# Optimization experiments

Hardware: AMD Instinct MI355X
Metric: run time of the kernel (lower is better)

Reference implementation:

```python
import jax, jax.numpy as jnp
import numpy as np

M = 16384      # total flat points per role (8 scenes x 2048 pts)
D = 256        # d_model
H = 4          # heads
K = 16         # knn neighbors
DFF = 1024     # 4*D
LN_EPS = 1e-5


def _ln(x, g, b):
    m = jnp.mean(x, axis=-1, keepdims=True)
    v = jnp.mean((x - m) ** 2, axis=-1, keepdims=True)
    return (x - m) / jnp.sqrt(v + LN_EPS) * g + b


def _knn_block(x, coord, ctx, ctx_coord, idx,
               Wq, Wk, Wv, Wo, g1, b1, pe_w, pe_b,
               W1, bf1, W2, bf2, g2, b2):
    # x: [M,D] query feats; ctx: [N,D] context feats; idx: [M,K] neighbor ids (-1 = invalid)
    m, d = x.shape
    k = idx.shape[1]
    dh = d // H
    valid = idx >= 0
    idx_c = jnp.where(valid, idx, 0)

    xn = _ln(x, g1, b1)
    q = (xn @ Wq).reshape(m, H, dh)                      # [M,H,dh]
    k_all = ctx @ Wk                                     # [N,D]
    v_all = ctx @ Wv                                     # [N,D]

    rel = coord[:, None, :] - ctx_coord[idx_c]           # [M,K,3]
    pe = rel @ pe_w + pe_b                               # [M,K,D] relative position encoding
    kg = (k_all[idx_c] + pe).reshape(m, k, H, dh)        # gathered keys  [M,K,H,dh]
    vg = (v_all[idx_c] + pe).reshape(m, k, H, dh)        # gathered values

    scale = jnp.asarray(1.0 / np.sqrt(dh), x.dtype)
    scores = jnp.einsum('mhd,mkhd->mhk', q, kg) * scale
    scores = jnp.where(valid[:, None, :], scores, jnp.asarray(-1e9, x.dtype))
    attn = jax.nn.softmax(scores, axis=-1)
    out = jnp.einsum('mhk,mkhd->mhd', attn, vg).reshape(m, d) @ Wo
    x = x + out
    h = jax.nn.gelu(_ln(x, g2, b2) @ W1 + bf1)
    return x + (h @ W2 + bf2)


def setup_inputs() -> dict:
    key = jax.random.key(0)
    ks = jax.random.split(key, 24)
    s = 0.02
    nblk = 2  # [0]=self(a), [1]=cross(a,b)
    inp = {
        'feat_a': jax.random.normal(ks[0], (M, D), jnp.float32),
        'coord_a': jax.random.normal(ks[1], (M, 3), jnp.float32),
        'feat_b': jax.random.normal(ks[2], (M, D), jnp.float32),
        'coord_b': jax.random.normal(ks[3], (M, 3), jnp.float32),
        'Wq': jax.random.normal(ks[4], (nblk, D, D), jnp.float32) * s,
        'Wk': jax.random.normal(ks[5], (nblk, D, D), jnp.float32) * s,
        'Wv': jax.random.normal(ks[6], (nblk, D, D), jnp.float32) * s,
        'Wo': jax.random.normal(ks[7], (nblk, D, D), jnp.float32) * s,
        'ln1_g': jnp.ones((nblk, D), jnp.float32),
        'ln1_b': jnp.zeros((nblk, D), jnp.float32),
        'pe_w': jax.random.normal(ks[8], (nblk, 3, D), jnp.float32) * s,
        'pe_b': jnp.zeros((nblk, D), jnp.float32),
        'ffn_w1': jax.random.normal(ks[9], (nblk, D, DFF), jnp.float32) * s,
        'ffn_b1': jnp.zeros((nblk, DFF), jnp.float32),
        'ffn_w2': jax.random.normal(ks[10], (nblk, DFF, D), jnp.float32) * s,
        'ffn_b2': jnp.zeros((nblk, D), jnp.float32),
        'ln2_g': jnp.ones((nblk, D), jnp.float32),
        'ln2_b': jnp.zeros((nblk, D), jnp.float32),
        'knn_a2a': jax.random.randint(ks[11], (M, K), 0, M, jnp.int64 if jax.config.jax_enable_x64 else jnp.int32),
        'knn_a2b': jax.random.randint(ks[12], (M, K), 0, M, jnp.int64 if jax.config.jax_enable_x64 else jnp.int32),
    }
    return inp


def reference(feat_a, coord_a, feat_b, coord_b,
              Wq, Wk, Wv, Wo, ln1_g, ln1_b, pe_w, pe_b,
              ffn_w1, ffn_b1, ffn_w2, ffn_b2, ln2_g, ln2_b,
              knn_a2a, knn_a2b):
    def params(i):
        return (Wq[i], Wk[i], Wv[i], Wo[i], ln1_g[i], ln1_b[i], pe_w[i], pe_b[i],
                ffn_w1[i], ffn_b1[i], ffn_w2[i], ffn_b2[i], ln2_g[i], ln2_b[i])
    # layer 'self(a)': feat[a] = block(feat[a], coord[a], knn_indexes['a2a'])
    fa = _knn_block(feat_a, coord_a, feat_a, coord_a, knn_a2a, *params(0))
    # layer 'cross(a,b)': feat[a] = block(query=feat[a], context=feat[b], knn_indexes['a2b'])
    fa = _knn_block(fa, coord_a, feat_b, coord_b, knn_a2b, *params(1))
    return fa
```

## Files before the change

### kernel.cpp

```cpp
#include <hip/hip_runtime.h>
#include <hip/hip_bf16.h>
#include <stdint.h>

#define MM 16384
#define DD 256
#define HH 4
#define KK 16
#define DFF_ 1024

typedef __attribute__((ext_vector_type(8))) short bf16x8;
typedef __attribute__((ext_vector_type(16))) float f32x16;
typedef __attribute__((ext_vector_type(2))) float f32x2;

__device__ __forceinline__ unsigned short f2bf(float f) {
    unsigned u = __builtin_bit_cast(unsigned, f);
    unsigned r = u + 0x7fffu + ((u >> 16) & 1u);
    return (unsigned short)(r >> 16);
}
__device__ __forceinline__ float bf2f(unsigned short h) {
    unsigned u = ((unsigned)h) << 16;
    return __builtin_bit_cast(float, u);
}


__global__ __launch_bounds__(256) void prep_weights(
        const float* __restrict__ Wq, const float* __restrict__ Wk,
        const float* __restrict__ Wv, const float* __restrict__ Wo,
        const float* __restrict__ W1, const float* __restrict__ W2,
        unsigned short* __restrict__ wf) {
    int t = blockIdx.x * blockDim.x + threadIdx.x;
    const float* src; unsigned short* dst;
    int kd, lg, rem, blk, e, sect;
    if (t < 131072) { sect = 0; rem = t; blk = rem >> 16; e = rem & 65535;
        src = Wq; dst = wf + blk * 65536; kd = 256; lg = 8; }
    else if (t < 262144) { sect = 1; rem = t - 131072; blk = rem >> 16; e = rem & 65535;
        src = Wk; dst = wf + 131072 + blk * 131072; kd = 256; lg = 8; }
    else if (t < 393216) { sect = 2; rem = t - 262144; blk = rem >> 16; e = rem & 65535;
        src = Wv; dst = wf + 131072 + blk * 131072; kd = 256; lg = 8; }
    else if (t < 524288) { sect = 0; rem = t - 393216; blk = rem >> 16; e = rem & 65535;
        src = Wo; dst = wf + 393216 + blk * 65536; kd = 256; lg = 8; }
    else if (t < 1048576) { sect = 0; rem = t - 524288; blk = rem >> 18; e = rem & 262143;
        src = W1; dst = wf + 524288 + blk * 262144; kd = 256; lg = 10; }
    else if (t < 1572864) { sect = 0; rem = t - 1048576; blk = rem >> 18; e = rem & 262143;
        src = W2; dst = wf + 1048576 + blk * 262144; kd = 1024; lg = 8; }
    else return;
    int k = e >> lg;
    int n = e & ((1 << lg) - 1);
    if (sect == 1) n = (n >> 2) * 8 + (n & 3);
    else if (sect == 2) n = (n >> 2) * 8 + 4 + (n & 3);
    float v = src[(size_t)blk * kd * (1 << lg) + e];
    int off = ((n >> 5) * (kd >> 4) + (k >> 4)) * 512 + (((k >> 3) & 1) * 32 + (n & 31)) * 8 + (k & 7);
    dst[off] = f2bf(v);
}

__global__ __launch_bounds__(256) void ln3_to_frag(
        const float* __restrict__ xa, const float* __restrict__ g,
        const float* __restrict__ b, const float* __restrict__ xb,
        unsigned short* __restrict__ outln, unsigned short* __restrict__ outca,
        unsigned short* __restrict__ outcb) {
    int y = blockIdx.y;
    const float* x = (y == 2) ? xb : xa;
    unsigned short* out = (y == 0) ? outln : (y == 1 ? outca : outcb);
    int apply_ln = (y == 0);
    int wave = threadIdx.x >> 6, lane = threadIdx.x & 63;
    int m = blockIdx.x * 4 + wave;
    const float4 xv = reinterpret_cast<const float4*>(x + (size_t)m * DD)[lane];
    float vals[4] = {xv.x, xv.y, xv.z, xv.w};
    int k0 = lane * 4;
    if (apply_ln) {
        float s = vals[0] + vals[1] + vals[2] + vals[3];
        float sq = vals[0]*vals[0] + vals[1]*vals[1] + vals[2]*vals[2] + vals[3]*vals[3];
        for (int o = 32; o; o >>= 1) { s += __shfl_xor(s, o, 64); sq += __shfl_xor(sq, o, 64); }
        float mean = s * (1.0f / DD);
        float var = sq * (1.0f / DD) - mean * mean;
        float rs = rsqrtf(var + 1e-5f);
        #pragma unroll
        for (int c = 0; c < 4; ++c)
            vals[c] = (vals[c] - mean) * rs * g[k0 + c] + b[k0 + c];
    }
    int chunk = ((m >> 5) * (DD >> 4) + (k0 >> 4)) * 64 + ((k0 >> 3) & 1) * 32 + (m & 31);
    ushort4 o4 = make_ushort4(f2bf(vals[0]), f2bf(vals[1]), f2bf(vals[2]), f2bf(vals[3]));
    *reinterpret_cast<ushort4*>(out + (size_t)chunk * 8 + (k0 & 7)) = o4;
}

template <int KG>
__device__ __forceinline__ void compute_tile(
        const bf16x8* __restrict__ a0, const bf16x8* __restrict__ a1,
        const bf16x8* __restrict__ b0, const bf16x8* __restrict__ b1,
        f32x16 acc[2][2]) {
    #pragma unroll 4
    for (int g = 0; g < KG; ++g) {
        bf16x8 av0 = a0[g * 64];
        bf16x8 av1 = a1[g * 64];
        bf16x8 bv0 = b0[g * 64];
        bf16x8 bv1 = b1[g * 64];
        acc[0][0] = __builtin_amdgcn_mfma_f32_32x32x16_bf16(av0, bv0, acc[0][0], 0, 0, 0);
        acc[0][1] = __builtin_amdgcn_mfma_f32_32x32x16_bf16(av0, bv1, acc[0][1], 0, 0, 0);
        acc[1][0] = __builtin_amdgcn_mfma_f32_32x32x16_bf16(av1, bv0, acc[1][0], 0, 0, 0);
        acc[1][1] = __builtin_amdgcn_mfma_f32_32x32x16_bf16(av1, bv1, acc[1][1], 0, 0, 0);
    }
}

template <int O, int N>
__device__ __forceinline__ void redstage(float* a, int lane) {
    int sel = lane & O;
    #pragma unroll
    for (int u = 0; u < N / 2; ++u) {
        float lo = a[2 * u], hi = a[2 * u + 1];
        float keep = sel ? hi : lo;
        float send = sel ? lo : hi;
        a[u] = keep + __shfl_xor(send, O, 64);
    }
}

__global__ __launch_bounds__(512) void wo_ln_ffn1(
        const bf16x8* __restrict__ A, const bf16x8* __restrict__ Bo,
        float* __restrict__ xmid, const float* __restrict__ resid,
        const float* __restrict__ lng, const float* __restrict__ lnb,
        const bf16x8* __restrict__ B1, const float* __restrict__ b1,
        unsigned short* __restrict__ geluf) {
    constexpr int KG = 16;
    __shared__ float pstat[4][64][2];
    __shared__ float stats[64][2];
    __shared__ float tlds[8][32 * 33];
    __shared__ alignas(16) unsigned short xnlds[2][16][64][8];
    int wave = threadIdx.x >> 6, lane = threadIdx.x & 63;
    int wm = wave >> 2, wn = wave & 3;
    int m0 = blockIdx.x * 64;
    int mw = m0 + wm * 32;
    int n0 = wn * 64;
    const bf16x8* a0 = A + ((size_t)(mw >> 5) * KG) * 64 + lane;
    const bf16x8* b0 = Bo + ((size_t)(n0 >> 5) * KG) * 64 + lane;
    const bf16x8* b1o = b0 + (size_t)KG * 64;
    f32x16 acc[2] = {};
    #pragma unroll 4
    for (int g = 0; g < KG; ++g) {
        bf16x8 av = a0[g * 64];
        bf16x8 bv0 = b0[g * 64];
        bf16x8 bv1 = b1o[g * 64];
        acc[0] = __builtin_amdgcn_mfma_f32_32x32x16_bf16(av, bv0, acc[0], 0, 0, 0);
        acc[1] = __builtin_amdgcn_mfma_f32_32x32x16_bf16(av, bv1, acc[1], 0, 0, 0);
    }
    int col = lane & 31, rq = (lane >> 5) * 4;

    #pragma unroll
    for (int j = 0; j < 2; ++j) {
        #pragma unroll
        for (int r = 0; r < 16; ++r) {
            int row = (r & 3) + 8 * (r >> 2) + rq;
            int m = mw + row;
            int n = n0 + j * 32 + col;
            float v = acc[j][r];
            v += resid[(size_t)m * DD + n];
            xmid[(size_t)m * DD + n] = v;
            acc[j][r] = v;
        }
    }

    {
        float ps[16];
        #pragma unroll
        for (int r = 0; r < 16; ++r) ps[r] = acc[0][r] + acc[1][r];
        redstage<1, 16>(ps, lane);
        redstage<2, 8>(ps, lane);
        redstage<4, 4>(ps, lane);
        redstage<8, 2>(ps, lane);
        float sum64 = ps[0] + __shfl_xor(ps[0], 16, 64);
        float qs[16];
        #pragma unroll
        for (int r = 0; r < 16; ++r) {
            float a = acc[0][r], b = acc[1][r];
            qs[r] = a * a + b * b;
        }
        redstage<1, 16>(qs, lane);
        redstage<2, 8>(qs, lane);
        redstage<4, 4>(qs, lane);
        redstage<8, 2>(qs, lane);
        float sq64 = qs[0] + __shfl_xor(qs[0], 16, 64);
        int slot = lane & 15;
        int ROW = wm * 32 + (slot & 3) + 8 * (slot >> 2) + rq;
        if ((lane & 16) == 0)
            *reinterpret_cast<float2*>(&pstat[wn][ROW][0]) = make_float2(sum64, sq64);
    }
    __syncthreads();
    if (threadIdx.x < 64) {
        int R = threadIdx.x;
        float s = 0.0f, sq = 0.0f;
        #pragma unroll
        for (int w = 0; w < 4; ++w) {
            float2 p = *reinterpret_cast<float2*>(&pstat[w][R][0]);
            s += p.x; sq += p.y;
        }
        float mean = s * (1.0f / DD);
        float var = sq * (1.0f / DD) - mean * mean;
        float rstd = rsqrtf(var + 1e-5f);
        *reinterpret_cast<float2*>(&stats[R][0]) = make_float2(mean, rstd);
    }
    __syncthreads();

    {
        float* wlds = &tlds[wave][0];
        float mean_r[16], rstd_r[16];
        #pragma unroll
        for (int r = 0; r < 16; ++r) {
            int row = (r & 3) + 8 * (r >> 2) + rq;
            float2 st = *reinterpret_cast<float2*>(&stats[wm * 32 + row][0]);
            mean_r[r] = st.x; rstd_r[r] = st.y;
        }
        for (int j = 0; j < 2; ++j) {
            float gj = lng[n0 + j * 32 + col];
            float bj = lnb[n0 + j * 32 + col];
            #pragma unroll
            for (int r = 0; r < 16; ++r) {
                int row = (r & 3) + 8 * (r >> 2) + rq;
                float v = (acc[j][r] - mean_r[r]) * rstd_r[r] * gj + bj;
                wlds[row * 33 + col] = v;
            }
            #pragma unroll
            for (int it = 0; it < 2; ++it) {
                int task = lane + it * 64;
                int row = task >> 2, cc = task & 3;
                int m = mw + row;
                int k = n0 + j * 32 + cc * 8;
                float* p = &wlds[row * 33 + cc * 8];
                unsigned short us[8];
                #pragma unroll
                for (int e = 0; e < 8; ++e) us[e] = f2bf(p[e]);
                int lch = (k >> 4) * 64 + ((k >> 3) & 1) * 32 + (m & 31);
                reinterpret_cast<uint4*>(&xnlds[wm][0][0][0])[lch] = *reinterpret_cast<uint4*>(us);
            }
        }
    }
    __syncthreads();

    const bf16x8* la = (const bf16x8*)&xnlds[wm][0][0][0] + lane;
    #pragma unroll
    for (int h = 0; h < 2; ++h) {
        int nw3 = h * 512 + wn * 128;
        const bf16x8* bb = B1 + ((size_t)(nw3 >> 5) * KG) * 64 + lane;
        f32x16 acc4[4] = {};
        #pragma unroll 4
        for (int g = 0; g < KG; ++g) {
            bf16x8 av = la[g * 64];
            bf16x8 bv0 = bb[g * 64];
            bf16x8 bv1 = bb[(KG + g) * 64];
            bf16x8 bv2 = bb[(2 * KG + g) * 64];
            bf16x8 bv3 = bb[(3 * KG + g) * 64];
            acc4[0] = __builtin_amdgcn_mfma_f32_32x32x16_bf16(av, bv0, acc4[0], 0, 0, 0);
            acc4[1] = __builtin_amdgcn_mfma_f32_32x32x16_bf16(av, bv1, acc4[1], 0, 0, 0);
            acc4[2] = __builtin_amdgcn_mfma_f32_32x32x16_bf16(av, bv2, acc4[2], 0, 0, 0);
            acc4[3] = __builtin_amdgcn_mfma_f32_32x32x16_bf16(av, bv3, acc4[3], 0, 0, 0);
        }
        float* wlds = &tlds[wave][0];
        for (int j = 0; j < 4; ++j) {
            #pragma unroll
            for (int r = 0; r < 16; ++r) {
                int row = (r & 3) + 8 * (r >> 2) + rq;
                int n = nw3 + j * 32 + col;
                float v = acc4[j][r] + b1[n];
                float arg = v * (1.5957691216f + 0.0713548163f * v * v);
                v = v * __frcp_rn(1.0f + __expf(-arg));
                wlds[row * 33 + col] = v;
            }
            #pragma unroll
            for (int it = 0; it < 2; ++it) {
                int task = lane + it * 64;
                int row = task >> 2, cc = task & 3;
                int m = mw + row;
                int k = nw3 + j * 32 + cc * 8;
                float* p = &wlds[row * 33 + cc * 8];
                unsigned short us[8];
                #pragma unroll
                for (int e = 0; e < 8; ++e) us[e] = f2bf(p[e]);
                int chunk = ((m >> 5) * (DFF_ >> 4) + (k >> 4)) * 64 + ((k >> 3) & 1) * 32 + (m & 31);
                reinterpret_cast<uint4*>(geluf)[chunk] = *reinterpret_cast<uint4*>(us);
            }
        }
    }
}

template <int KD, int NOUT, bool RESID, bool BIAS>
__global__ __launch_bounds__(256) void gemm_frag64(
        const bf16x8* __restrict__ A, const bf16x8* __restrict__ B,
        float* __restrict__ outp, const float* __restrict__ resid,
        const float* __restrict__ bias) {
    constexpr int KG = KD / 16;
    int wave = threadIdx.x >> 6, lane = threadIdx.x & 63;
    int wm = wave & 1, wn = wave >> 1;
    int mw = blockIdx.x * 64 + wm * 32;
    int nw = blockIdx.y * 128 + wn * 64;
    const bf16x8* a0 = A + ((size_t)(mw >> 5) * KG) * 64 + lane;
    const bf16x8* b0 = B + ((size_t)(nw >> 5) * KG) * 64 + lane;
    const bf16x8* b1 = b0 + (size_t)KG * 64;
    f32x16 acc[2] = {};
    #pragma unroll 4
    for (int g = 0; g < KG; ++g) {
        bf16x8 av = a0[g * 64];
        bf16x8 bv0 = b0[g * 64];
        bf16x8 bv1 = b1[g * 64];
        acc[0] = __builtin_amdgcn_mfma_f32_32x32x16_bf16(av, bv0, acc[0], 0, 0, 0);
        acc[1] = __builtin_amdgcn_mfma_f32_32x32x16_bf16(av, bv1, acc[1], 0, 0, 0);
    }
    int col = lane & 31, rq = (lane >> 5) * 4;
    #pragma unroll
    for (int j = 0; j < 2; ++j) {
        #pragma unroll
        for (int r = 0; r < 16; ++r) {
            int row = (r & 3) + 8 * (r >> 2) + rq;
            int m = mw + row;
            int n = nw + j * 32 + col;
            float v = acc[j][r];
            if (BIAS) v += bias[n];
            if (RESID) v += resid[(size_t)m * NOUT + n];
            outp[(size_t)m * NOUT + n] = v;
        }
    }
}

__global__ __launch_bounds__(256) void gemm_qkv(
        const bf16x8* __restrict__ Aq, const bf16x8* __restrict__ Akv,
        const bf16x8* __restrict__ Bq, const bf16x8* __restrict__ Bkv,
        unsigned short* __restrict__ qout, unsigned char* __restrict__ kvout) {
    constexpr int KG = 16;
    int wave = threadIdx.x >> 6, lane = threadIdx.x & 63;
    int wm = wave & 1, wn = wave >> 1;
    int y = blockIdx.y;
    bool isQ = y < 2;
    const bf16x8* A = isQ ? Aq : Akv;
    const bf16x8* B = isQ ? Bq : Bkv;
    int n0 = (isQ ? y : y - 2) * 128 + wn * 64;
    int m0 = blockIdx.x * 128 + wm * 64;
    const bf16x8* a0 = A + ((size_t)(m0 >> 5) * KG) * 64 + lane;
    const bf16x8* a1 = a0 + (size_t)KG * 64;
    const bf16x8* b0 = B + ((size_t)(n0 >> 5) * KG) * 64 + lane;
    const bf16x8* b1 = b0 + (size_t)KG * 64;
    f32x16 acc[2][2] = {};
    compute_tile<KG>(a0, a1, b0, b1, acc);
    int col = lane & 31, rq = (lane >> 5) * 4;
    #pragma unroll
    for (int i = 0; i < 2; ++i)
    #pragma unroll
    for (int j = 0; j < 2; ++j)
    #pragma unroll
    for (int r = 0; r < 16; ++r) {
        int row = (r & 3) + 8 * (r >> 2) + rq;
        int m = m0 + i * 32 + row;
        int n = n0 + j * 32 + col;
        float v = acc[i][j][r];
        if (isQ) qout[(size_t)m * 256 + n] = f2bf(v);
        else kvout[(size_t)m * 512 + n] =
            (unsigned char)(__builtin_amdgcn_cvt_pk_fp8_f32(v, v, 0, false) & 0xff);
    }
}

template <int KD, bool BIAS>
__global__ __launch_bounds__(512) void gemm_ln(
        const bf16x8* __restrict__ A, const bf16x8* __restrict__ B,
        float* __restrict__ out_f32, const float* __restrict__ resid,
        const float* __restrict__ bias,
        const float* __restrict__ lng, const float* __restrict__ lnb,
        unsigned short* __restrict__ out_frag) {
    constexpr int KG = KD / 16;
    __shared__ float pstat[4][64][2];
    __shared__ float stats[64][2];
    __shared__ float tlds[8][32 * 33];
    int wave = threadIdx.x >> 6, lane = threadIdx.x & 63;
    int wm = wave >> 2, wn = wave & 3;
    int m0 = blockIdx.x * 64;
    int mw = m0 + wm * 32;
    int n0 = wn * 64;
    const bf16x8* a0 = A + ((size_t)(mw >> 5) * KG) * 64 + lane;
    const bf16x8* b0 = B + ((size_t)(n0 >> 5) * KG) * 64 + lane;
    const bf16x8* b1 = b0 + (size_t)KG * 64;
    f32x16 acc[2] = {};
    #pragma unroll 4
    for (int g = 0; g < KG; ++g) {
        bf16x8 av = a0[g * 64];
        bf16x8 bv0 = b0[g * 64];
        bf16x8 bv1 = b1[g * 64];
        acc[0] = __builtin_amdgcn_mfma_f32_32x32x16_bf16(av, bv0, acc[0], 0, 0, 0);
        acc[1] = __builtin_amdgcn_mfma_f32_32x32x16_bf16(av, bv1, acc[1], 0, 0, 0);
    }
    int col = lane & 31, rq = (lane >> 5) * 4;

    #pragma unroll
    for (int j = 0; j < 2; ++j) {
        #pragma unroll
        for (int r = 0; r < 16; ++r) {
            int row = (r & 3) + 8 * (r >> 2) + rq;
            int m = mw + row;
            int n = n0 + j * 32 + col;
            float v = acc[j][r];
            if (BIAS) v += bias[n];
            v += resid[(size_t)m * DD + n];
            out_f32[(size_t)m * DD + n] = v;
            acc[j][r] = v;
        }
    }

    {
        float ps[16];
        #pragma unroll
        for (int r = 0; r < 16; ++r)
            ps[r] = acc[0][r] + acc[1][r];
        redstage<1, 16>(ps, lane);
        redstage<2, 8>(ps, lane);
        redstage<4, 4>(ps, lane);
        redstage<8, 2>(ps, lane);
        float sum64 = ps[0] + __shfl_xor(ps[0], 16, 64);
        float qs[16];
        #pragma unroll
        for (int r = 0; r < 16; ++r) {
            float a = acc[0][r], b = acc[1][r];
            qs[r] = a * a + b * b;
        }
        redstage<1, 16>(qs, lane);
        redstage<2, 8>(qs, lane);
        redstage<4, 4>(qs, lane);
        redstage<8, 2>(qs, lane);
        float sq64 = qs[0] + __shfl_xor(qs[0], 16, 64);
        int slot = lane & 15;
        int ROW = wm * 32 + (slot & 3) + 8 * (slot >> 2) + rq;
        if ((lane & 16) == 0)
            *reinterpret_cast<float2*>(&pstat[wn][ROW][0]) = make_float2(sum64, sq64);
    }
    __syncthreads();
    if (threadIdx.x < 64) {
        int R = threadIdx.x;
        float s = 0.0f, sq = 0.0f;
        #pragma unroll
        for (int w = 0; w < 4; ++w) {
            float2 p = *reinterpret_cast<float2*>(&pstat[w][R][0]);
            s += p.x; sq += p.y;
        }
        float mean = s * (1.0f / DD);
        float var = sq * (1.0f / DD) - mean * mean;
        float rstd = rsqrtf(var + 1e-5f);
        *reinterpret_cast<float2*>(&stats[R][0]) = make_float2(mean, rstd);
    }
    __syncthreads();

    float* wlds = &tlds[wave][0];
    float mean_r[16], rstd_r[16];
    #pragma unroll
    for (int r = 0; r < 16; ++r) {
        int row = (r & 3) + 8 * (r >> 2) + rq;
        float2 st = *reinterpret_cast<float2*>(&stats[wm * 32 + row][0]);
        mean_r[r] = st.x; rstd_r[r] = st.y;
    }
    for (int j = 0; j < 2; ++j) {
        float gj = lng[n0 + j * 32 + col];
        float bj = lnb[n0 + j * 32 + col];
        #pragma unroll
        for (int r = 0; r < 16; ++r) {
            int row = (r & 3) + 8 * (r >> 2) + rq;
            float v = (acc[j][r] - mean_r[r]) * rstd_r[r] * gj + bj;
            wlds[row * 33 + col] = v;
        }
        #pragma unroll
        for (int it = 0; it < 2; ++it) {
            int task = lane + it * 64;
            int row = task >> 2, cc = task & 3;
            int m = mw + row;
            int k = n0 + j * 32 + cc * 8;
            float* p = &wlds[row * 33 + cc * 8];
            unsigned short us[8];
            #pragma unroll
            for (int e = 0; e < 8; ++e) us[e] = f2bf(p[e]);
            int chunk = ((m >> 5) * (DD >> 4) + (k >> 4)) * 64 + ((k >> 3) & 1) * 32 + (m & 31);
            *reinterpret_cast<uint4*>(out_frag + (size_t)chunk * 8) = *reinterpret_cast<uint4*>(us);
        }
    }
}

__global__ __launch_bounds__(256) void attn_kernel(
        const unsigned short* __restrict__ q, const unsigned char* __restrict__ kv,
        const float* __restrict__ coord, const float* __restrict__ ctx_coord,
        const int* __restrict__ knn,
        const float* __restrict__ pe_w, const float* __restrict__ pe_b,
        unsigned short* __restrict__ out_frag) {
    int wave = threadIdx.x >> 6, lane = threadIdx.x & 63;
    int m = blockIdx.x * 4 + wave;
    int s = lane & 15;
    int d0 = (lane >> 4) * 64 + s * 4;

    ushort4 qv4 = *reinterpret_cast<const ushort4*>(q + (size_t)m * DD + d0);
    float qx = bf2f(qv4.x), qy = bf2f(qv4.y), qz = bf2f(qv4.z), qw = bf2f(qv4.w);
    float4 pw0 = *reinterpret_cast<const float4*>(pe_w + d0);
    float4 pw1 = *reinterpret_cast<const float4*>(pe_w + DD + d0);
    float4 pw2 = *reinterpret_cast<const float4*>(pe_w + 2 * DD + d0);
    float4 pbv = *reinterpret_cast<const float4*>(pe_b + d0);

    float cx = coord[m * 3], cy = coord[m * 3 + 1], cz = coord[m * 3 + 2];
    int myidx = knn[(size_t)m * KK + s];
    int icm = myidx < 0 ? 0 : myidx;
    float rx = cx - ctx_coord[icm * 3];
    float ry = cy - ctx_coord[icm * 3 + 1];
    float rz = cz - ctx_coord[icm * 3 + 2];

    float t0 = qx * pw0.x + qy * pw0.y + qz * pw0.z + qw * pw0.w;
    float t1 = qx * pw1.x + qy * pw1.y + qz * pw1.z + qw * pw1.w;
    float t2 = qx * pw2.x + qy * pw2.y + qz * pw2.z + qw * pw2.w;
    float t3 = qx * pbv.x + qy * pbv.y + qz * pbv.z + qw * pbv.w;
// ... 63 lines not shown
    aw += wrx * pw0.w + wry * pw1.w + wrz * pw2.w + pbv.w;

    ushort4 o4 = make_ushort4(f2bf(ax), f2bf(ay), f2bf(az), f2bf(aw));
    int chunk = ((m >> 5) * (DD >> 4) + (d0 >> 4)) * 64 + ((d0 >> 3) & 1) * 32 + (m & 31);
    *reinterpret_cast<ushort4*>(out_frag + (size_t)chunk * 8 + (d0 & 7)) = o4;
}

extern "C" void kernel_launch(void* const* d_in, const int* in_sizes, int n_in,
                              void* d_out, int out_size, void* d_ws, size_t ws_size,
                              hipStream_t stream) {
    const float* feat_a = (const float*)d_in[0];
    const float* coord_a = (const float*)d_in[1];
    const float* feat_b = (const float*)d_in[2];
    const float* coord_b = (const float*)d_in[3];
    const float* Wq = (const float*)d_in[4];
    const float* Wk = (const float*)d_in[5];
    const float* Wv = (const float*)d_in[6];
    const float* Wo = (const float*)d_in[7];
    const float* ln1_g = (const float*)d_in[8];
    const float* ln1_b = (const float*)d_in[9];
    const float* pe_w = (const float*)d_in[10];
    const float* pe_b = (const float*)d_in[11];
    const float* W1 = (const float*)d_in[12];
    const float* b1 = (const float*)d_in[13];
    const float* W2 = (const float*)d_in[14];
    const float* b2 = (const float*)d_in[15];
    const float* ln2_g = (const float*)d_in[16];
    const float* ln2_b = (const float*)d_in[17];
    const int* knn_a2a = (const int*)d_in[18];
    const int* knn_a2b = (const int*)d_in[19];

    char* ws = (char*)d_ws;
    unsigned short* wfrag = (unsigned short*)ws;
    float* xmid = (float*)(ws + (4ull << 20));
    float* xout0 = (float*)(ws + (20ull << 20));
    unsigned short* qbuf = (unsigned short*)(ws + (36ull << 20));
    unsigned char* kvbuf = (unsigned char*)(ws + (52ull << 20));
    unsigned short* xnf = (unsigned short*)(ws + (68ull << 20));
    unsigned short* ctxfa = (unsigned short*)(ws + (76ull << 20));
    unsigned short* attnf = (unsigned short*)(ws + (84ull << 20));
    unsigned short* ctxfb = (unsigned short*)(ws + (92ull << 20));
    unsigned short* geluf = (unsigned short*)(ws + (36ull << 20));

    const unsigned short* WQF = wfrag;
    const unsigned short* KVF = wfrag + 131072;
    const unsigned short* WOF = wfrag + 393216;
    const unsigned short* W1F = wfrag + 524288;
    const unsigned short* W2F = wfrag + 1048576;

    prep_weights<<<(1572864 + 255) / 256, 256, 0, stream>>>(Wq, Wk, Wv, Wo, W1, W2, wfrag);

    ln3_to_frag<<<dim3(MM / 4, 3), 256, 0, stream>>>(feat_a, ln1_g, ln1_b, feat_b,
                                                     xnf, ctxfa, ctxfb);

    gemm_qkv<<<dim3(MM / 128, 6), 256, 0, stream>>>(
        (const bf16x8*)xnf, (const bf16x8*)ctxfa,
        (const bf16x8*)WQF, (const bf16x8*)KVF, qbuf, kvbuf);

    attn_kernel<<<MM / 4, 256, 0, stream>>>(qbuf, kvbuf, coord_a, coord_a, knn_a2a,
                                            pe_w, pe_b, attnf);

    wo_ln_ffn1<<<MM / 64, 512, 0, stream>>>(
        (const bf16x8*)attnf, (const bf16x8*)WOF, xmid, feat_a,
        ln2_g, ln2_b, (const bf16x8*)W1F, b1, geluf);

    gemm_ln<1024, true><<<MM / 64, 512, 0, stream>>>(
        (const bf16x8*)geluf, (const bf16x8*)W2F, xout0, xmid, b2,
        ln1_g + DD, ln1_b + DD, xnf);

    gemm_qkv<<<dim3(MM / 128, 6), 256, 0, stream>>>(
        (const bf16x8*)xnf, (const bf16x8*)ctxfb,
        (const bf16x8*)(WQF + 65536), (const bf16x8*)(KVF + 131072), qbuf, kvbuf);

    attn_kernel<<<MM / 4, 256, 0, stream>>>(qbuf, kvbuf, coord_a, coord_b, knn_a2b,
                                            pe_w + 3 * DD, pe_b + DD, attnf);

    wo_ln_ffn1<<<MM / 64, 512, 0, stream>>>(
        (const bf16x8*)attnf, (const bf16x8*)(WOF + 65536), xmid, xout0,
        ln2_g + DD, ln2_b + DD, (const bf16x8*)(W1F + 262144), b1 + DFF_, geluf);

    gemm_frag64<1024, 256, true, true><<<dim3(MM / 64, 2), 256, 0, stream>>>(
        (const bf16x8*)geluf, (const bf16x8*)(W2F + 262144), (float*)d_out, xmid,
        b2 + DD);
}
```

Measured before the change: 313.1 us.

## Fuse Wo, LN2, FFN1 and FFN2 into one kernel using FP8 FFN weights

Merges the Wo projection, residual add, LN2, the W1 GEMM with GELU, the W2 GEMM and the next block's LN1 into a single kernel per block. The GELU activations now stay in shared memory as FP8, so the global geluf and xmid round trips and two launches go away. The FFN weights are pre-quantised to FP8 with power-of-two scales and run through fp8 MFMA instructions. gemm_qkv also gets an XCD-aware block index remap. Risks include lower numerical precision from FP8, and heavy shared memory use (about 80 KB per block) that limits occupancy.

Result: faster. 292.9 us (-6.5%).

```diff
diff --git a/kernel.cpp b/kernel.cpp
--- a/kernel.cpp
+++ b/kernel.cpp
@@ -29,7 +29,7 @@
         const float* __restrict__ W1, const float* __restrict__ W2,
         unsigned short* __restrict__ wf) {
     int t = blockIdx.x * blockDim.x + threadIdx.x;
-    const float* src; unsigned short* dst;
+    const float* src; unsigned short* dst = nullptr;
     int kd, lg, rem, blk, e, sect;
     if (t < 131072) { sect = 0; rem = t; blk = rem >> 16; e = rem & 65535;
         src = Wq; dst = wf + blk * 65536; kd = 256; lg = 8; }
@@ -39,10 +39,10 @@
         src = Wv; dst = wf + 131072 + blk * 131072; kd = 256; lg = 8; }
     else if (t < 524288) { sect = 0; rem = t - 393216; blk = rem >> 16; e = rem & 65535;
         src = Wo; dst = wf + 393216 + blk * 65536; kd = 256; lg = 8; }
-    else if (t < 1048576) { sect = 0; rem = t - 524288; blk = rem >> 18; e = rem & 262143;
-        src = W1; dst = wf + 524288 + blk * 262144; kd = 256; lg = 10; }
-    else if (t < 1572864) { sect = 0; rem = t - 1048576; blk = rem >> 18; e = rem & 262143;
-        src = W2; dst = wf + 1048576 + blk * 262144; kd = 1024; lg = 8; }
+    else if (t < 1048576) { sect = 3; rem = t - 524288; blk = rem >> 18; e = rem & 262143;
+        src = W1; kd = 256; lg = 10; }
+    else if (t < 1572864) { sect = 4; rem = t - 1048576; blk = rem >> 18; e = rem & 262143;
+        src = W2; kd = 1024; lg = 8; }
     else return;
     int k = e >> lg;
     int n = e & ((1 << lg) - 1);
@@ -50,7 +50,17 @@
     else if (sect == 2) n = (n >> 2) * 8 + 4 + (n & 3);
     float v = src[(size_t)blk * kd * (1 << lg) + e];
     int off = ((n >> 5) * (kd >> 4) + (k >> 4)) * 512 + (((k >> 3) & 1) * 32 + (n & 31)) * 8 + (k & 7);
-    dst[off] = f2bf(v);
+    if (sect == 3) {
+        unsigned char* d8 = ((unsigned char*)wf) + 3145728 + blk * 262144;
+        float vs = v * 32.0f;
+        d8[off] = (unsigned char)(__builtin_amdgcn_cvt_pk_fp8_f32(vs, vs, 0, false) & 0xff);
+    } else if (sect == 4) {
+        unsigned char* d8 = ((unsigned char*)wf) + 3670016 + blk * 262144;
+        float vs = v * 16.0f;
+        d8[off] = (unsigned char)(__builtin_amdgcn_cvt_pk_fp8_f32(vs, vs, 0, false) & 0xff);
+    } else {
+        dst[off] = f2bf(v);
+    }
 }
 
 __global__ __launch_bounds__(256) void ln3_to_frag(
@@ -101,222 +111,6 @@
     }
 }
 
-template <int O, int N>
-__device__ __forceinline__ void redstage(float* a, int lane) {
-    int sel = lane & O;
-    #pragma unroll
-    for (int u = 0; u < N / 2; ++u) {
-        float lo = a[2 * u], hi = a[2 * u + 1];
-        float keep = sel ? hi : lo;
-        float send = sel ? lo : hi;
-        a[u] = keep + __shfl_xor(send, O, 64);
-    }
-}
-
-__global__ __launch_bounds__(512) void wo_ln_ffn1(
-        const bf16x8* __restrict__ A, const bf16x8* __restrict__ Bo,
-        float* __restrict__ xmid, const float* __restrict__ resid,
-        const float* __restrict__ lng, const float* __restrict__ lnb,
-        const bf16x8* __restrict__ B1, const float* __restrict__ b1,
-        unsigned short* __restrict__ geluf) {
-    constexpr int KG = 16;
-    __shared__ float pstat[4][64][2];
-    __shared__ float stats[64][2];
-    __shared__ float tlds[8][32 * 33];
-    __shared__ alignas(16) unsigned short xnlds[2][16][64][8];
-    int wave = threadIdx.x >> 6, lane = threadIdx.x & 63;
-    int wm = wave >> 2, wn = wave & 3;
-    int m0 = blockIdx.x * 64;
-    int mw = m0 + wm * 32;
-    int n0 = wn * 64;
-    const bf16x8* a0 = A + ((size_t)(mw >> 5) * KG) * 64 + lane;
-    const bf16x8* b0 = Bo + ((size_t)(n0 >> 5) * KG) * 64 + lane;
-    const bf16x8* b1o = b0 + (size_t)KG * 64;
-    f32x16 acc[2] = {};
-    #pragma unroll 4
-    for (int g = 0; g < KG; ++g) {
-        bf16x8 av = a0[g * 64];
-        bf16x8 bv0 = b0[g * 64];
-        bf16x8 bv1 = b1o[g * 64];
-        acc[0] = __builtin_amdgcn_mfma_f32_32x32x16_bf16(av, bv0, acc[0], 0, 0, 0);
-        acc[1] = __builtin_amdgcn_mfma_f32_32x32x16_bf16(av, bv1, acc[1], 0, 0, 0);
-    }
-    int col = lane & 31, rq = (lane >> 5) * 4;
-
-    #pragma unroll
-    for (int j = 0; j < 2; ++j) {
-        #pragma unroll
-        for (int r = 0; r < 16; ++r) {
-            int row = (r & 3) + 8 * (r >> 2) + rq;
-            int m = mw + row;
-            int n = n0 + j * 32 + col;
-            float v = acc[j][r];
-            v += resid[(size_t)m * DD + n];
-            xmid[(size_t)m * DD + n] = v;
-            acc[j][r] = v;
-        }
-    }
-
-    {
-        float ps[16];
-        #pragma unroll
-        for (int r = 0; r < 16; ++r) ps[r] = acc[0][r] + acc[1][r];
-        redstage<1, 16>(ps, lane);
-        redstage<2, 8>(ps, lane);
-        redstage<4, 4>(ps, lane);
-        redstage<8, 2>(ps, lane);
-        float sum64 = ps[0] + __shfl_xor(ps[0], 16, 64);
-        float qs[16];
-        #pragma unroll
-        for (int r = 0; r < 16; ++r) {
-            float a = acc[0][r], b = acc[1][r];
-            qs[r] = a * a + b * b;
-        }
-        redstage<1, 16>(qs, lane);
-        redstage<2, 8>(qs, lane);
-        redstage<4, 4>(qs, lane);
-        redstage<8, 2>(qs, lane);
-        float sq64 = qs[0] + __shfl_xor(qs[0], 16, 64);
-        int slot = lane & 15;
-        int ROW = wm * 32 + (slot & 3) + 8 * (slot >> 2) + rq;
-        if ((lane & 16) == 0)
-            *reinterpret_cast<float2*>(&pstat[wn][ROW][0]) = make_float2(sum64, sq64);
-    }
-    __syncthreads();
-    if (threadIdx.x < 64) {
-        int R = threadIdx.x;
-        float s = 0.0f, sq = 0.0f;
-        #pragma unroll
-        for (int w = 0; w < 4; ++w) {
-            float2 p = *reinterpret_cast<float2*>(&pstat[w][R][0]);
-            s += p.x; sq += p.y;
-        }
-        float mean = s * (1.0f / DD);
-        float var = sq * (1.0f / DD) - mean * mean;
-        float rstd = rsqrtf(var + 1e-5f);
-        *reinterpret_cast<float2*>(&stats[R][0]) = make_float2(mean, rstd);
-    }
-    __syncthreads();
-
-    {
-        float* wlds = &tlds[wave][0];
-        float mean_r[16], rstd_r[16];
-        #pragma unroll
-        for (int r = 0; r < 16; ++r) {
-            int row = (r & 3) + 8 * (r >> 2) + rq;
-            float2 st = *reinterpret_cast<float2*>(&stats[wm * 32 + row][0]);
-            mean_r[r] = st.x; rstd_r[r] = st.y;
-        }
-        for (int j = 0; j < 2; ++j) {
-            float gj = lng[n0 + j * 32 + col];
-            float bj = lnb[n0 + j * 32 + col];
-            #pragma unroll
-            for (int r = 0; r < 16; ++r) {
-                int row = (r & 3) + 8 * (r >> 2) + rq;
-                float v = (acc[j][r] - mean_r[r]) * rstd_r[r] * gj + bj;
-                wlds[row * 33 + col] = v;
-            }
-            #pragma unroll
-            for (int it = 0; it < 2; ++it) {
-                int task = lane + it * 64;
-                int row = task >> 2, cc = task & 3;
-                int m = mw + row;
-                int k = n0 + j * 32 + cc * 8;
-                float* p = &wlds[row * 33 + cc * 8];
-                unsigned short us[8];
-                #pragma unroll
-                for (int e = 0; e < 8; ++e) us[e] = f2bf(p[e]);
-                int lch = (k >> 4) * 64 + ((k >> 3) & 1) * 32 + (m & 31);
-                reinterpret_cast<uint4*>(&xnlds[wm][0][0][0])[lch] = *reinterpret_cast<uint4*>(us);
-            }
-        }
-    }
-    __syncthreads();
-
-    const bf16x8* la = (const bf16x8*)&xnlds[wm][0][0][0] + lane;
-    #pragma unroll
-    for (int h = 0; h < 2; ++h) {
-        int nw3 = h * 512 + wn * 128;
-        const bf16x8* bb = B1 + ((size_t)(nw3 >> 5) * KG) * 64 + lane;
-        f32x16 acc4[4] = {};
-        #pragma unroll 4
-        for (int g = 0; g < KG; ++g) {
-            bf16x8 av = la[g * 64];
-            bf16x8 bv0 = bb[g * 64];
-            bf16x8 bv1 = bb[(KG + g) * 64];
-            bf16x8 bv2 = bb[(2 * KG + g) * 64];
-            bf16x8 bv3 = bb[(3 * KG + g) * 64];
-            acc4[0] = __builtin_amdgcn_mfma_f32_32x32x16_bf16(av, bv0, acc4[0], 0, 0, 0);
-            acc4[1] = __builtin_amdgcn_mfma_f32_32x32x16_bf16(av, bv1, acc4[1], 0, 0, 0);
-            acc4[2] = __builtin_amdgcn_mfma_f32_32x32x16_bf16(av, bv2, acc4[2], 0, 0, 0);
-            acc4[3] = __builtin_amdgcn_mfma_f32_32x32x16_bf16(av, bv3, acc4[3], 0, 0, 0);
-        }
-        float* wlds = &tlds[wave][0];
-        for (int j = 0; j < 4; ++j) {
-            #pragma unroll
-            for (int r = 0; r < 16; ++r) {
-                int row = (r & 3) + 8 * (r >> 2) + rq;
-                int n = nw3 + j * 32 + col;
-                float v = acc4[j][r] + b1[n];
-                float arg = v * (1.5957691216f + 0.0713548163f * v * v);
-                v = v * __frcp_rn(1.0f + __expf(-arg));
-                wlds[row * 33 + col] = v;
-            }
-            #pragma unroll
-            for (int it = 0; it < 2; ++it) {
-                int task = lane + it * 64;
-                int row = task >> 2, cc = task & 3;
-                int m = mw + row;
-                int k = nw3 + j * 32 + cc * 8;
-                float* p = &wlds[row * 33 + cc * 8];
-                unsigned short us[8];
-                #pragma unroll
-                for (int e = 0; e < 8; ++e) us[e] = f2bf(p[e]);
-                int chunk = ((m >> 5) * (DFF_ >> 4) + (k >> 4)) * 64 + ((k >> 3) & 1) * 32 + (m & 31);
-                reinterpret_cast<uint4*>(geluf)[chunk] = *reinterpret_cast<uint4*>(us);
-            }
-        }
-    }
-}
-
-template <int KD, int NOUT, bool RESID, bool BIAS>
-__global__ __launch_bounds__(256) void gemm_frag64(
-        const bf16x8* __restrict__ A, const bf16x8* __restrict__ B,
-        float* __restrict__ outp, const float* __restrict__ resid,
-        const float* __restrict__ bias) {
-    constexpr int KG = KD / 16;
-    int wave = threadIdx.x >> 6, lane = threadIdx.x & 63;
-    int wm = wave & 1, wn = wave >> 1;
-    int mw = blockIdx.x * 64 + wm * 32;
-    int nw = blockIdx.y * 128 + wn * 64;
-    const bf16x8* a0 = A + ((size_t)(mw >> 5) * KG) * 64 + lane;
-    const bf16x8* b0 = B + ((size_t)(nw >> 5) * KG) * 64 + lane;
-    const bf16x8* b1 = b0 + (size_t)KG * 64;
-    f32x16 acc[2] = {};
-    #pragma unroll 4
-    for (int g = 0; g < KG; ++g) {
-        bf16x8 av = a0[g * 64];
-        bf16x8 bv0 = b0[g * 64];
-        bf16x8 bv1 = b1[g * 64];
-        acc[0] = __builtin_amdgcn_mfma_f32_32x32x16_bf16(av, bv0, acc[0], 0, 0, 0);
-        acc[1] = __builtin_amdgcn_mfma_f32_32x32x16_bf16(av, bv1, acc[1], 0, 0, 0);
-    }
-    int col = lane & 31, rq = (lane >> 5) * 4;
-    #pragma unroll
-    for (int j = 0; j < 2; ++j) {
-        #pragma unroll
-        for (int r = 0; r < 16; ++r) {
-            int row = (r & 3) + 8 * (r >> 2) + rq;
-            int m = mw + row;
-            int n = nw + j * 32 + col;
-            float v = acc[j][r];
-            if (BIAS) v += bias[n];
-            if (RESID) v += resid[(size_t)m * NOUT + n];
-            outp[(size_t)m * NOUT + n] = v;
-        }
-    }
-}
-
 __global__ __launch_bounds__(256) void gemm_qkv(
         const bf16x8* __restrict__ Aq, const bf16x8* __restrict__ Akv,
         const bf16x8* __restrict__ Bq, const bf16x8* __restrict__ Bkv,
@@ -324,12 +118,15 @@
     constexpr int KG = 16;
     int wave = threadIdx.x >> 6, lane = threadIdx.x & 63;
     int wm = wave & 1, wn = wave >> 1;
-    int y = blockIdx.y;
+    int id = blockIdx.x;
+    int xcd = id & 7, slot = id >> 3;
+    int bx = 16 * xcd + (slot & 15);
+    int y = slot >> 4;
     bool isQ = y < 2;
     const bf16x8* A = isQ ? Aq : Akv;
     const bf16x8* B = isQ ? Bq : Bkv;
     int n0 = (isQ ? y : y - 2) * 128 + wn * 64;
-    int m0 = blockIdx.x * 128 + wm * 64;
+    int m0 = bx * 128 + wm * 64;
     const bf16x8* a0 = A + ((size_t)(m0 >> 5) * KG) * 64 + lane;
     const bf16x8* a1 = a0 + (size_t)KG * 64;
     const bf16x8* b0 = B + ((size_t)(n0 >> 5) * KG) * 64 + lane;
@@ -353,122 +150,298 @@
     }
 }
 
-template <int KD, bool BIAS>
-__global__ __launch_bounds__(512) void gemm_ln(
-        const bf16x8* __restrict__ A, const bf16x8* __restrict__ B,
-        float* __restrict__ out_f32, const float* __restrict__ resid,
-        const float* __restrict__ bias,
-        const float* __restrict__ lng, const float* __restrict__ lnb,
-        unsigned short* __restrict__ out_frag) {
-    constexpr int KG = KD / 16;
+template <int O, int N>
+__device__ __forceinline__ void redstage(float* a, int lane) {
+    int sel = lane & O;
+    #pragma unroll
+    for (int u = 0; u < N / 2; ++u) {
+        float lo = a[2 * u], hi = a[2 * u + 1];
+        float keep = sel ? hi : lo;
+        float send = sel ? lo : hi;
+        a[u] = keep + __shfl_xor(send, O, 64);
+    }
+}
+
+template <bool TAIL>
+__global__ __launch_bounds__(512) void mega_tail(
+        const bf16x8* __restrict__ A, const bf16x8* __restrict__ Bo,
+        const float* __restrict__ resid,
+        const float* __restrict__ ln2g, const float* __restrict__ ln2b,
+        const unsigned char* __restrict__ B1_8, const float* __restrict__ b1,
+        const unsigned char* __restrict__ B2_8, const float* __restrict__ b2,
+        const float* __restrict__ ln1g, const float* __restrict__ ln1b,
+        float* __restrict__ xout, unsigned short* __restrict__ xnf_out) {
+    constexpr int KG = 16;
     __shared__ float pstat[4][64][2];
     __shared__ float stats[64][2];
     __shared__ float tlds[8][32 * 33];
+    __shared__ alignas(16) unsigned char xn8[2][8192];
+    __shared__ alignas(16) unsigned char gelu8[2][32768];
     int wave = threadIdx.x >> 6, lane = threadIdx.x & 63;
     int wm = wave >> 2, wn = wave & 3;
     int m0 = blockIdx.x * 64;
     int mw = m0 + wm * 32;
-    int n0 = wn * 64;
-    const bf16x8* a0 = A + ((size_t)(mw >> 5) * KG) * 64 + lane;
-    const bf16x8* b0 = B + ((size_t)(n0 >> 5) * KG) * 64 + lane;
-    const bf16x8* b1 = b0 + (size_t)KG * 64;
-    f32x16 acc[2] = {};
-    #pragma unroll 4
-    for (int g = 0; g < KG; ++g) {
-        bf16x8 av = a0[g * 64];
-        bf16x8 bv0 = b0[g * 64];
-        bf16x8 bv1 = b1[g * 64];
-        acc[0] = __builtin_amdgcn_mfma_f32_32x32x16_bf16(av, bv0, acc[0], 0, 0, 0);
-        acc[1] = __builtin_amdgcn_mfma_f32_32x32x16_bf16(av, bv1, acc[1], 0, 0, 0);
-    }
     int col = lane & 31, rq = (lane >> 5) * 4;
 
-    #pragma unroll
-    for (int j = 0; j < 2; ++j) {
+    f32x16 xm[2];
+    {
+        int n0 = wn * 64;
+        const bf16x8* a0 = A + ((size_t)(mw >> 5) * KG) * 64 + lane;
+        const bf16x8* b0 = Bo + ((size_t)(n0 >> 5) * KG) * 64 + lane;
+        const bf16x8* b1o = b0 + (size_t)KG * 64;
+        f32x16 acc[2] = {};
+        #pragma unroll 4
+        for (int g = 0; g < KG; ++g) {
+            bf16x8 av = a0[g * 64];
+            bf16x8 bv0 = b0[g * 64];
+            bf16x8 bv1 = b1o[g * 64];
+            acc[0] = __builtin_amdgcn_mfma_f32_32x32x16_bf16(av, bv0, acc[0], 0, 0, 0);
+            acc[1] = __builtin_amdgcn_mfma_f32_32x32x16_bf16(av, bv1, acc[1], 0, 0, 0);
+        }
+        #pragma unroll
+        for (int j = 0; j < 2; ++j)
         #pragma unroll
         for (int r = 0; r < 16; ++r) {
             int row = (r & 3) + 8 * (r >> 2) + rq;
             int m = mw + row;
             int n = n0 + j * 32 + col;
-            float v = acc[j][r];
-            if (BIAS) v += bias[n];
-            v += resid[(size_t)m * DD + n];
-            out_f32[(size_t)m * DD + n] = v;
-            acc[j][r] = v;
-        }
-    }
-
-    {
-        float ps[16];
-        #pragma unroll
-        for (int r = 0; r < 16; ++r)
-            ps[r] = acc[0][r] + acc[1][r];
-        redstage<1, 16>(ps, lane);
-        redstage<2, 8>(ps, lane);
-        redstage<4, 4>(ps, lane);
-        redstage<8, 2>(ps, lane);
-        float sum64 = ps[0] + __shfl_xor(ps[0], 16, 64);
-        float qs[16];
-        #pragma unroll
-        for (int r = 0; r < 16; ++r) {
-            float a = acc[0][r], b = acc[1][r];
-            qs[r] = a * a + b * b;
-        }
-        redstage<1, 16>(qs, lane);
-        redstage<2, 8>(qs, lane);
-        redstage<4, 4>(qs, lane);
-        redstage<8, 2>(qs, lane);
-        float sq64 = qs[0] + __shfl_xor(qs[0], 16, 64);
-        int slot = lane & 15;
-        int ROW = wm * 32 + (slot & 3) + 8 * (slot >> 2) + rq;
-        if ((lane & 16) == 0)
-            *reinterpret_cast<float2*>(&pstat[wn][ROW][0]) = make_float2(sum64, sq64);
-    }
-    __syncthreads();
-    if (threadIdx.x < 64) {
-        int R = threadIdx.x;
-        float s = 0.0f, sq = 0.0f;
-        #pragma unroll
-        for (int w = 0; w < 4; ++w) {
-            float2 p = *reinterpret_cast<float2*>(&pstat[w][R][0]);
-            s += p.x; sq += p.y;
-        }
-        float mean = s * (1.0f / DD);
-        float var = sq * (1.0f / DD) - mean * mean;
-        float rstd = rsqrtf(var + 1e-5f);
-        *reinterpret_cast<float2*>(&stats[R][0]) = make_float2(mean, rstd);
-    }
-    __syncthreads();
-
-    float* wlds = &tlds[wave][0];
-    float mean_r[16], rstd_r[16];
-    #pragma unroll
-    for (int r = 0; r < 16; ++r) {
-        int row = (r & 3) + 8 * (r >> 2) + rq;
-        float2 st = *reinterpret_cast<float2*>(&stats[wm * 32 + row][0]);
-        mean_r[r] = st.x; rstd_r[r] = st.y;
-    }
-    for (int j = 0; j < 2; ++j) {
-        float gj = lng[n0 + j * 32 + col];
-        float bj = lnb[n0 + j * 32 + col];
+            xm[j][r] = acc[j][r] + resid[(size_t)m * DD + n];
+        }
+        {
+            float ps[16];
+            #pragma unroll
+            for (int r = 0; r < 16; ++r) ps[r] = xm[0][r] + xm[1][r];
+            redstage<1, 16>(ps, lane);
+            redstage<2, 8>(ps, lane);
+            redstage<4, 4>(ps, lane);
+            redstage<8, 2>(ps, lane);
+            float sum64 = ps[0] + __shfl_xor(ps[0], 16, 64);
+            float qs[16];
+            #pragma unroll
+            for (int r = 0; r < 16; ++r) {
+                float a2 = xm[0][r], b2v = xm[1][r];
+                qs[r] = a2 * a2 + b2v * b2v;
+            }
+            redstage<1, 16>(qs, lane);
+            redstage<2, 8>(qs, lane);
+            redstage<4, 4>(qs, lane);
+            redstage<8, 2>(qs, lane);
+            float sq64 = qs[0] + __shfl_xor(qs[0], 16, 64);
+            int slot = lane & 15;
+            int ROW = wm * 32 + (slot & 3) + 8 * (slot >> 2) + rq;
+            if ((lane & 16) == 0)
+                *reinterpret_cast<float2*>(&pstat[wn][ROW][0]) = make_float2(sum64, sq64);
+        }
+        __syncthreads();
+        if (threadIdx.x < 64) {
+            int R = threadIdx.x;
+            float s = 0.0f, sq = 0.0f;
+            #pragma unroll
+            for (int w = 0; w < 4; ++w) {
+                float2 p = *reinterpret_cast<float2*>(&pstat[w][R][0]);
+                s += p.x; sq += p.y;
+            }
+            float mean = s * (1.0f / DD);
+            float var = sq * (1.0f / DD) - mean * mean;
+            float rstd = rsqrtf(var + 1e-5f);
+            *reinterpret_cast<float2*>(&stats[R][0]) = make_float2(mean, rstd);
+        }
+        __syncthreads();
+        float* wlds = &tlds[wave][0];
+        float mean_r[16], rstd_r[16];
         #pragma unroll
         for (int r = 0; r < 16; ++r) {
             int row = (r & 3) + 8 * (r >> 2) + rq;
-            float v = (acc[j][r] - mean_r[r]) * rstd_r[r] * gj + bj;
-            wlds[row * 33 + col] = v;
-        }
+            float2 st = *reinterpret_cast<float2*>(&stats[wm * 32 + row][0]);
+            mean_r[r] = st.x; rstd_r[r] = st.y;
+        }
+        for (int j = 0; j < 2; ++j) {
+            float gj = ln2g[n0 + j * 32 + col];
+            float bj = ln2b[n0 + j * 32 + col];
+            #pragma unroll
+            for (int r = 0; r < 16; ++r) {
+                int row = (r & 3) + 8 * (r >> 2) + rq;
+                float v = (xm[j][r] - mean_r[r]) * rstd_r[r] * gj + bj;
+                wlds[row * 33 + col] = v;
+            }
+            #pragma unroll
+            for (int it = 0; it < 2; ++it) {
+                int task = lane + it * 64;
+                int row = task >> 2, cc = task & 3;
+                int k = n0 + j * 32 + cc * 8;
+                float* p = &wlds[row * 33 + cc * 8];
+                unsigned w0 = __builtin_amdgcn_cvt_pk_fp8_f32(p[0], p[1], 0, false);
+                w0 = __builtin_amdgcn_cvt_pk_fp8_f32(p[2], p[3], w0, true);
+                unsigned w1 = __builtin_amdgcn_cvt_pk_fp8_f32(p[4], p[5], 0, false);
+                w1 = __builtin_amdgcn_cvt_pk_fp8_f32(p[6], p[7], w1, true);
+                int lch = (k >> 4) * 64 + ((k >> 3) & 1) * 32 + row;
+                *reinterpret_cast<uint2*>(&xn8[wm][lch * 8]) = make_uint2(w0, w1);
+            }
+        }
+    }
+    __syncthreads();
+
+    {
+        const unsigned char* la8 = &xn8[wm][lane * 8];
         #pragma unroll
-        for (int it = 0; it < 2; ++it) {
-            int task = lane + it * 64;
-            int row = task >> 2, cc = task & 3;
-            int m = mw + row;
-            int k = n0 + j * 32 + cc * 8;
-            float* p = &wlds[row * 33 + cc * 8];
-            unsigned short us[8];
-            #pragma unroll
-            for (int e = 0; e < 8; ++e) us[e] = f2bf(p[e]);
-            int chunk = ((m >> 5) * (DD >> 4) + (k >> 4)) * 64 + ((k >> 3) & 1) * 32 + (m & 31);
-            *reinterpret_cast<uint4*>(out_frag + (size_t)chunk * 8) = *reinterpret_cast<uint4*>(us);
+        for (int h = 0; h < 2; ++h) {
+            int nw2 = h * 512 + wn * 128;
+            const uint2* bb = (const uint2*)B1_8 + ((size_t)(nw2 >> 5) * KG) * 64 + lane;
+            f32x16 acc4[4] = {};
+            #pragma unroll 2
+            for (int g = 0; g < KG; ++g) {
+                long av = __builtin_bit_cast(long, *reinterpret_cast<const uint2*>(la8 + g * 512));
+                long bv0 = __builtin_bit_cast(long, bb[g * 64]);
+                long bv1 = __builtin_bit_cast(long, bb[(KG + g) * 64]);
+                long bv2 = __builtin_bit_cast(long, bb[(2 * KG + g) * 64]);
+                long bv3 = __builtin_bit_cast(long, bb[(3 * KG + g) * 64]);
+                acc4[0] = __builtin_amdgcn_mfma_f32_32x32x16_fp8_fp8(av, bv0, acc4[0], 0, 0, 0);
+                acc4[1] = __builtin_amdgcn_mfma_f32_32x32x16_fp8_fp8(av, bv1, acc4[1], 0, 0, 0);
+                acc4[2] = __builtin_amdgcn_mfma_f32_32x32x16_fp8_fp8(av, bv2, acc4[2], 0, 0, 0);
+                acc4[3] = __builtin_amdgcn_mfma_f32_32x32x16_fp8_fp8(av, bv3, acc4[3], 0, 0, 0);
+            }
+            float* wlds = &tlds[wave][0];
+            for (int j = 0; j < 4; ++j) {
+                #pragma unroll
+                for (int r = 0; r < 16; ++r) {
+                    int row = (r & 3) + 8 * (r >> 2) + rq;
+                    int n = nw2 + j * 32 + col;
+                    float v = acc4[j][r] * (1.0f / 32.0f) + b1[n];
+                    float arg = v * (1.5957691216f + 0.0713548163f * v * v);
+                    v = v * __frcp_rn(1.0f + __expf(-arg));
+                    wlds[row * 33 + col] = v;
+                }
+                #pragma unroll
+                for (int it = 0; it < 2; ++it) {
+                    int task = lane + it * 64;
+                    int row = task >> 2, cc = task & 3;
+                    int k = nw2 + j * 32 + cc * 8;
+                    float* p = &wlds[row * 33 + cc * 8];
+                    unsigned w0 = __builtin_amdgcn_cvt_pk_fp8_f32(p[0] * 16.f, p[1] * 16.f, 0, false);
+                    w0 = __builtin_amdgcn_cvt_pk_fp8_f32(p[2] * 16.f, p[3] * 16.f, w0, true);
+                    unsigned w1 = __builtin_amdgcn_cvt_pk_fp8_f32(p[4] * 16.f, p[5] * 16.f, 0, false);
+                    w1 = __builtin_amdgcn_cvt_pk_fp8_f32(p[6] * 16.f, p[7] * 16.f, w1, true);
+                    int lch = (k >> 4) * 64 + ((k >> 3) & 1) * 32 + row;
+                    *reinterpret_cast<uint2*>(&gelu8[wm][lch * 8]) = make_uint2(w0, w1);
+                }
+            }
+        }
+    }
+    __syncthreads();
+
+    {
+        constexpr int KG2 = 64;
+        int n0 = wn * 64;
+        const unsigned char* lg8 = &gelu8[wm][lane * 8];
+        const uint2* bp0 = (const uint2*)B2_8 + ((size_t)(n0 >> 5) * KG2) * 64 + lane;
+        const uint2* bp1 = bp0 + (size_t)KG2 * 64;
+        f32x16 acc[2] = {};
+        #pragma unroll 4
+        for (int g = 0; g < KG2; ++g) {
+            long av = __builtin_bit_cast(long, *reinterpret_cast<const uint2*>(lg8 + g * 512));
+            long bv0 = __builtin_bit_cast(long, bp0[g * 64]);
+            long bv1 = __builtin_bit_cast(long, bp1[g * 64]);
+            acc[0] = __builtin_amdgcn_mfma_f32_32x32x16_fp8_fp8(av, bv0, acc[0], 0, 0, 0);
+            acc[1] = __builtin_amdgcn_mfma_f32_32x32x16_fp8_fp8(av, bv1, acc[1], 0, 0, 0);
+        }
+        #pragma unroll
+        for (int j = 0; j < 2; ++j)
+        #pragma unroll
+        for (int r = 0; r < 16; ++r) {
+            int n = n0 + j * 32 + col;
+            acc[j][r] = acc[j][r] * (1.0f / 256.0f) + b2[n] + xm[j][r];
+        }
+        if constexpr (TAIL) {
+            #pragma unroll
+            for (int j = 0; j < 2; ++j)
+            #pragma unroll
+            for (int r = 0; r < 16; ++r) {
+                int row = (r & 3) + 8 * (r >> 2) + rq;
+                int m = mw + row;
+                int n = n0 + j * 32 + col;
+                xout[(size_t)m * DD + n] = acc[j][r];
+            }
+        } else {
+            #pragma unroll
+            for (int j = 0; j < 2; ++j)
+            #pragma unroll
+            for (int r = 0; r < 16; ++r) {
+                int row = (r & 3) + 8 * (r >> 2) + rq;
+                int m = mw + row;
+                int n = n0 + j * 32 + col;
+                xout[(size_t)m * DD + n] = acc[j][r];
+            }
+            {
+                float ps[16];
+                #pragma unroll
+                for (int r = 0; r < 16; ++r) ps[r] = acc[0][r] + acc[1][r];
+                redstage<1, 16>(ps, lane);
+                redstage<2, 8>(ps, lane);
+                redstage<4, 4>(ps, lane);
+                redstage<8, 2>(ps, lane);
+                float sum64 = ps[0] + __shfl_xor(ps[0], 16, 64);
+                float qs[16];
+                #pragma unroll
+                for (int r = 0; r < 16; ++r) {
+                    float a2 = acc[0][r], b2v = acc[1][r];
+                    qs[r] = a2 * a2 + b2v * b2v;
+                }
+                redstage<1, 16>(qs, lane);
+                redstage<2, 8>(qs, lane);
+                redstage<4, 4>(qs, lane);
+                redstage<8, 2>(qs, lane);
+                float sq64 = qs[0] + __shfl_xor(qs[0], 16, 64);
+                int slot = lane & 15;
+                int ROW = wm * 32 + (slot & 3) + 8 * (slot >> 2) + rq;
+                if ((lane & 16) == 0)
+                    *reinterpret_cast<float2*>(&pstat[wn][ROW][0]) = make_float2(sum64, sq64);
+            }
+            __syncthreads();
+            if (threadIdx.x < 64) {
+                int R = threadIdx.x;
+                float s = 0.0f, sq = 0.0f;
+                #pragma unroll
+                for (int w = 0; w < 4; ++w) {
+                    float2 p = *reinterpret_cast<float2*>(&pstat[w][R][0]);
+                    s += p.x; sq += p.y;
+                }
+                float mean = s * (1.0f / DD);
+                float var = sq * (1.0f / DD) - mean * mean;
+                float rstd = rsqrtf(var + 1e-5f);
+                *reinterpret_cast<float2*>(&stats[R][0]) = make_float2(mean, rstd);
+            }
+            __syncthreads();
+            float* wlds = &tlds[wave][0];
+            float mean_r[16], rstd_r[16];
+            #pragma unroll
+            for (int r = 0; r < 16; ++r) {
+                int row = (r & 3) + 8 * (r >> 2) + rq;
+                float2 st = *reinterpret_cast<float2*>(&stats[wm * 32 + row][0]);
+                mean_r[r] = st.x; rstd_r[r] = st.y;
+            }
+            for (int j = 0; j < 2; ++j) {
+                float gj = ln1g[n0 + j * 32 + col];
+                float bj = ln1b[n0 + j * 32 + col];
+                #pragma unroll
+                for (int r = 0; r < 16; ++r) {
+                    int row = (r & 3) + 8 * (r >> 2) + rq;
+                    float v = (acc[j][r] - mean_r[r]) * rstd_r[r] * gj + bj;
+                    wlds[row * 33 + col] = v;
+                }
+                #pragma unroll
+                for (int it = 0; it < 2; ++it) {
+                    int task = lane + it * 64;
+                    int row = task >> 2, cc = task & 3;
+                    int m = mw + row;
+                    int k = n0 + j * 32 + cc * 8;
+                    float* p = &wlds[row * 33 + cc * 8];
+                    unsigned short us[8];
+                    #pragma unroll
+                    for (int e = 0; e < 8; ++e) us[e] = f2bf(p[e]);
+                    int chunk = ((m >> 5) * (DD >> 4) + (k >> 4)) * 64 + ((k >> 3) & 1) * 32 + (m & 31);
+                    *reinterpret_cast<uint4*>(xnf_out + (size_t)chunk * 8) = *reinterpret_cast<uint4*>(us);
+                }
+            }
         }
     }
 }
@@ -598,7 +571,6 @@
 
     char* ws = (char*)d_ws;
     unsigned short* wfrag = (unsigned short*)ws;
-    float* xmid = (float*)(ws + (4ull << 20));
     float* xout0 = (float*)(ws + (20ull << 20));
     unsigned short* qbuf = (unsigned short*)(ws + (36ull << 20));
     unsigned char* kvbuf = (unsigned char*)(ws + (52ull << 20));
@@ -606,46 +578,38 @@
     unsigned short* ctxfa = (unsigned short*)(ws + (76ull << 20));
     unsigned short* attnf = (unsigned short*)(ws + (84ull << 20));
     unsigned short* ctxfb = (unsigned short*)(ws + (92ull << 20));
-    unsigned short* geluf = (unsigned short*)(ws + (36ull << 20));
 
     const unsigned short* WQF = wfrag;
     const unsigned short* KVF = wfrag + 131072;
     const unsigned short* WOF = wfrag + 393216;
-    const unsigned short* W1F = wfrag + 524288;
-    const unsigned short* W2F = wfrag + 1048576;
+    const unsigned char* W1F8 = ((const unsigned char*)wfrag) + 3145728;
+    const unsigned char* W2F8 = ((const unsigned char*)wfrag) + 3670016;
 
     prep_weights<<<(1572864 + 255) / 256, 256, 0, stream>>>(Wq, Wk, Wv, Wo, W1, W2, wfrag);
 
     ln3_to_frag<<<dim3(MM / 4, 3), 256, 0, stream>>>(feat_a, ln1_g, ln1_b, feat_b,
                                                      xnf, ctxfa, ctxfb);
 
-    gemm_qkv<<<dim3(MM / 128, 6), 256, 0, stream>>>(
+    gemm_qkv<<<768, 256, 0, stream>>>(
         (const bf16x8*)xnf, (const bf16x8*)ctxfa,
         (const bf16x8*)WQF, (const bf16x8*)KVF, qbuf, kvbuf);
 
     attn_kernel<<<MM / 4, 256, 0, stream>>>(qbuf, kvbuf, coord_a, coord_a, knn_a2a,
                                             pe_w, pe_b, attnf);
 
-    wo_ln_ffn1<<<MM / 64, 512, 0, stream>>>(
-        (const bf16x8*)attnf, (const bf16x8*)WOF, xmid, feat_a,
-        ln2_g, ln2_b, (const bf16x8*)W1F, b1, geluf);
-
-    gemm_ln<1024, true><<<MM / 64, 512, 0, stream>>>(
-        (const bf16x8*)geluf, (const bf16x8*)W2F, xout0, xmid, b2,
-        ln1_g + DD, ln1_b + DD, xnf);
-
-    gemm_qkv<<<dim3(MM / 128, 6), 256, 0, stream>>>(
+    mega_tail<false><<<MM / 64, 512, 0, stream>>>(
+        (const bf16x8*)attnf, (const bf16x8*)WOF, feat_a, ln2_g, ln2_b,
+        W1F8, b1, W2F8, b2, ln1_g + DD, ln1_b + DD, xout0, xnf);
+
+    gemm_qkv<<<768, 256, 0, stream>>>(
         (const bf16x8*)xnf, (const bf16x8*)ctxfb,
         (const bf16x8*)(WQF + 65536), (const bf16x8*)(KVF + 131072), qbuf, kvbuf);
 
     attn_kernel<<<MM / 4, 256, 0, stream>>>(qbuf, kvbuf, coord_a, coord_b, knn_a2b,
                                             pe_w + 3 * DD, pe_b + DD, attnf);
 
-    wo_ln_ffn1<<<MM / 64, 512, 0, stream>>>(
-        (const bf16x8*)attnf, (const bf16x8*)(WOF + 65536), xmid, xout0,
-        ln2_g + DD, ln2_b + DD, (const bf16x8*)(W1F + 262144), b1 + DFF_, geluf);
-
-    gemm_frag64<1024, 256, true, true><<<dim3(MM / 64, 2), 256, 0, stream>>>(
-        (const bf16x8*)geluf, (const bf16x8*)(W2F + 262144), (float*)d_out, xmid,
-        b2 + DD);
-}
+    mega_tail<true><<<MM / 64, 512, 0, stream>>>(
+        (const bf16x8*)attnf, (const bf16x8*)(WOF + 65536), xout0,
+        ln2_g + DD, ln2_b + DD, W1F8 + 262144, b1 + DFF_,
+        W2F8 + 262144, b2 + DD, nullptr, nullptr, (float*)d_out, nullptr);
+}
```
